# Kernel tuning notes

Hardware: AMD Instinct MI355X
Metric: run time of the kernel (lower is better)

Reference implementation:

```python
import jax, jax.numpy as jnp
import numpy as np

N_EDGES = 262144
N_TRIP = 1048576
D = 128
N_RBF = 6
A_DIM = 49  # n_spher * l_spher
N_BIL = 8


def setup_inputs() -> dict:
    key = jax.random.key(0)
    ks = jax.random.split(key, 16)
    s = lambda fan_in: 1.0 / np.sqrt(fan_in)
    return {
        "m_ji": jax.random.normal(ks[0], (N_EDGES, D), jnp.float32),
        "e_rbf": jax.random.normal(ks[1], (N_EDGES, N_RBF), jnp.float32),
        "a_sbf": jax.random.normal(ks[2], (N_TRIP, A_DIM), jnp.float32),
        "nbr_list": jax.random.randint(ks[3], (N_EDGES, 2), 0, 100000),
        "angle_list": jax.random.randint(ks[4], (N_TRIP, 3), 0, N_EDGES),
        "kj_idx": jax.random.randint(ks[5], (N_TRIP,), 0, N_EDGES),
        "nbr_m_w": jax.random.normal(ks[6], (D, D), jnp.float32) * s(D),
        "nbr_m_b": jnp.zeros((D,), jnp.float32),
        "e_rbf_w": jax.random.normal(ks[7], (N_RBF, D), jnp.float32) * s(N_RBF),
        "a_sbf_w": jax.random.normal(ks[8], (A_DIM, N_BIL), jnp.float32) * s(A_DIM),
        "final_w": jax.random.normal(ks[9], (D, N_BIL, D), jnp.float32) * s(N_BIL * D),
        "m_ji_w": jax.random.normal(ks[10], (D, D), jnp.float32) * s(D),
        "m_ji_b": jnp.zeros((D,), jnp.float32),
        "post_w": jax.random.normal(ks[11], (D, D), jnp.float32) * s(D),
        "post_b": jnp.zeros((D,), jnp.float32),
        "res_w": jax.random.normal(ks[12], (3, 2, D, D), jnp.float32) * s(D),
        "res_b": jnp.zeros((3, 2, D), jnp.float32),
    }


def _residual(x, w2, b2):
    # two Dense(swish) layers + skip
    out = x
    for k in range(2):
        out = jax.nn.silu(out @ w2[k] + b2[k])
    return out + x


def reference(m_ji, e_rbf, a_sbf, nbr_list, angle_list, kj_idx,
              nbr_m_w, nbr_m_b, e_rbf_w, a_sbf_w, final_w,
              m_ji_w, m_ji_b, post_w, post_b, res_w, res_b):
    # DirectedMessage: gather per-triplet edge features
    t_m = jax.nn.silu(m_ji[kj_idx] @ nbr_m_w + nbr_m_b)   # [W, D]
    t_e = e_rbf[kj_idx] @ e_rbf_w                          # [W, D]
    m_and_e = t_m * t_e                                    # [W, D]
    t_a = a_sbf @ a_sbf_w                                  # [W, J]
    out = jnp.einsum('wj,wl,ijl->wi', t_a, m_and_e, final_w)  # [W, D]
    directed = jax.ops.segment_sum(out, kj_idx, num_segments=m_ji.shape[0])  # [E, D]

    transf_m_ji = jax.nn.silu(m_ji @ m_ji_w + m_ji_b)
    output = directed + transf_m_ji
    output = _residual(output, res_w[0], res_b[0])
    output = jax.nn.silu(output @ post_w + post_b) + transf_m_ji
    output = _residual(output, res_w[1], res_b[1])
    output = _residual(output, res_w[2], res_b[2])
    return output
```

## Files before the change

### kernel.cpp

```cpp
#include <hip/hip_runtime.h>

#define N_EDGE 262144
#define N_TRI  1048576
#define DIM    128
#define NRBF   6
#define ADIM   49
#define NBIL   8
#define TE     64
#define NTHR   256
#define SXD    68
#define EB2    2048
#define NSL    4

typedef __attribute__((ext_vector_type(8))) short bf16x8;
typedef __attribute__((ext_vector_type(4))) float f32x4;

__device__ __forceinline__ float fast_rcp(float x) {
    float r; asm("v_rcp_f32 %0, %1" : "=v"(r) : "v"(x)); return r;
}
__device__ __forceinline__ float fast_exp2(float x) {
    float r; asm("v_exp_f32 %0, %1" : "=v"(r) : "v"(x)); return r;
}
__device__ __forceinline__ float silu_f(float x) {
    return x * fast_rcp(1.f + fast_exp2(-1.44269504f * x));
}
__device__ __forceinline__ unsigned short f2bf(float f) {
    unsigned int u = __float_as_uint(f);
    return (unsigned short)((u + 0x7FFFu + ((u >> 16) & 1u)) >> 16);
}
__device__ __forceinline__ unsigned int pk2(float x, float y) {
    unsigned int r;
    asm("v_cvt_pk_bf16_f32 %0, %1, %2" : "=v"(r) : "v"(x), "v"(y));
    return r;
}
__device__ __forceinline__ float bf2f(unsigned short u) {
    return __uint_as_float(((unsigned int)u) << 16);
}

__global__ __launch_bounds__(256) void prep_w_k(
    const float* __restrict__ nbr, const float* __restrict__ mji,
    const float* __restrict__ post, const float* __restrict__ res,
    const float* __restrict__ fw, unsigned short* __restrict__ wt)
{
    int idx = blockIdx.x * 256 + threadIdx.x;
    if (idx < 9 * 16384) {
        int m = idx >> 14, rr = idx & 16383;
        int n = rr >> 7, ks = rr & 127;
        int ko = (ks & ~31) | ((ks & 1) << 4) | ((ks >> 1) & 15);
        const float* src = (m == 0) ? nbr : (m == 1) ? mji : (m == 2) ? post
                          : (res + (size_t)(m - 3) * 16384);
        wt[idx] = f2bf(src[ko * DIM + n]);
    } else {
        int r2 = idx - 9 * 16384;
        int n = r2 >> 10, j = (r2 >> 7) & 7, ls = r2 & 127;
        int lo = (ls & ~31) | ((ls & 1) << 4) | ((ls >> 1) & 15);
        wt[idx] = f2bf(fw[(size_t)(n * NBIL + j) * DIM + lo]);
    }
}

__global__ __launch_bounds__(256) void ta_all_k(
    const float* __restrict__ a_sbf, const float* __restrict__ a_sbf_w,
    float* __restrict__ taw)
{
    __shared__ __align__(16) float sA[256 * ADIM];
    __shared__ float sWa[ADIM * NBIL];
    const int tid = threadIdx.x;
    const size_t w0 = (size_t)blockIdx.x * 256;

    {
        const float4* src = (const float4*)(a_sbf + w0 * ADIM);
        float4* dst = (float4*)sA;
        for (int i = tid; i < (256 * ADIM) / 4; i += 256) dst[i] = src[i];
    }
    for (int i = tid; i < ADIM * NBIL; i += 256) sWa[i] = a_sbf_w[i];
    __syncthreads();

    float ta[NBIL];
    #pragma unroll
    for (int j = 0; j < NBIL; ++j) ta[j] = 0.0f;
    const float* row = sA + tid * ADIM;
    #pragma unroll
    for (int k = 0; k < ADIM; ++k) {
        float v = row[k];
        #pragma unroll
        for (int j = 0; j < NBIL; ++j) ta[j] = fmaf(v, sWa[k * NBIL + j], ta[j]);
    }
    float4* dst = (float4*)(taw + (w0 + tid) * NBIL);
    dst[0] = make_float4(ta[0], ta[1], ta[2], ta[3]);
    dst[1] = make_float4(ta[4], ta[5], ta[6], ta[7]);
}

__global__ __launch_bounds__(1024) void seg_reduce_k(
    const float* __restrict__ taw, const int* __restrict__ kj_idx,
    float* __restrict__ ta_sum)
{
    __shared__ float acc[EB2 * NBIL];
    const int tid = threadIdx.x;
    const int eg = blockIdx.x >> 2;
    const int sl = blockIdx.x & 3;
    const int lo = eg * EB2;

    for (int i = tid; i < EB2 * NBIL; i += 1024) acc[i] = 0.f;
    __syncthreads();

    const int4* kj4 = (const int4*)kj_idx;
    const int i0 = sl * (N_TRI / 4 / NSL);
    const int i1 = i0 + (N_TRI / 4 / NSL);
    for (int i = i0 + tid; i < i1; i += 1024) {
        int4 v = kj4[i];
        int w0 = i * 4;
        #pragma unroll
        for (int k = 0; k < 4; ++k) {
            int e = (k == 0) ? v.x : (k == 1) ? v.y : (k == 2) ? v.z : v.w;
            unsigned d = (unsigned)(e - lo);
            if (d < (unsigned)EB2) {
                const float4* p = (const float4*)(taw + (size_t)(w0 + k) * NBIL);
                float4 a = p[0], b = p[1];
                float* q = acc + d * NBIL;
                atomicAdd(q + 0, a.x); atomicAdd(q + 1, a.y);
                atomicAdd(q + 2, a.z); atomicAdd(q + 3, a.w);
                atomicAdd(q + 4, b.x); atomicAdd(q + 5, b.y);
                atomicAdd(q + 6, b.z); atomicAdd(q + 7, b.w);
            }
        }
    }
    __syncthreads();
    for (int i = tid; i < EB2 * NBIL; i += 1024)
        unsafeAtomicAdd(ta_sum + (size_t)lo * NBIL + i, acc[i]);
}

__global__ __launch_bounds__(256) void triplet_atomic_k(
    const float* __restrict__ a_sbf, const float* __restrict__ a_sbf_w,
    const int* __restrict__ kj_idx, float* __restrict__ ta_sum)
{
    __shared__ __align__(16) float sA[256 * ADIM];
    __shared__ float sWa[ADIM * NBIL];
    const int tid = threadIdx.x;
    const size_t w0 = (size_t)blockIdx.x * 256;
    {
        const float4* src = (const float4*)(a_sbf + w0 * ADIM);
        float4* dst = (float4*)sA;
        for (int i = tid; i < (256 * ADIM) / 4; i += 256) dst[i] = src[i];
    }
    for (int i = tid; i < ADIM * NBIL; i += 256) sWa[i] = a_sbf_w[i];
    __syncthreads();
    float ta[NBIL];
    #pragma unroll
    for (int j = 0; j < NBIL; ++j) ta[j] = 0.0f;
    const float* row = sA + tid * ADIM;
    #pragma unroll
    for (int k = 0; k < ADIM; ++k) {
        float v = row[k];
        #pragma unroll
        for (int j = 0; j < NBIL; ++j) ta[j] = fmaf(v, sWa[k * NBIL + j], ta[j]);
    }
    const int e = kj_idx[w0 + tid];
    float* dst = ta_sum + (size_t)e * NBIL;
    #pragma unroll
    for (int j = 0; j < NBIL; ++j) unsafeAtomicAdd(dst + j, ta[j]);
}

__global__ __launch_bounds__(NTHR) void edge_main_k(
    const float* __restrict__ m_ji, const float* __restrict__ e_rbf,
    const float* __restrict__ ta_sum, const unsigned short* __restrict__ wt,
    const float* __restrict__ nbr_m_b, const float* __restrict__ e_rbf_w,
    const float* __restrict__ m_ji_b, const float* __restrict__ post_b,
    const float* __restrict__ res_b, float* __restrict__ out)
{
    __shared__ __align__(16) unsigned int sXd[TE * SXD];
    __shared__ __align__(16) unsigned int sTd[TE * SXD];
    __shared__ __align__(16) float sTAT[NBIL * TE];
    __shared__ __align__(16) float sET[NRBF * TE];

    const int tid  = threadIdx.x;
    const int lane = tid & 63;
    const int ml   = lane & 15;
    const int g    = lane >> 4;
    const int wq   = tid >> 6;
    const int n0   = wq * 32;
    const int q16  = wq * 16;
    const size_t e0 = (size_t)blockIdx.x * TE;

    bf16x8 A[4][2], Bf[2][4];
    f32x4 acc[4][2], xr[4][2], zac;
    float b0, b1;

    auto prefB = [&](const unsigned short* wtm, int ldk, int kbase) {
        #pragma unroll
        for (int nt = 0; nt < 2; ++nt) {
            const unsigned short* wb =
                wtm + (size_t)(n0 + nt * 16 + ml) * ldk + kbase + g * 8;
            #pragma unroll
            for (int ks = 0; ks < 4; ++ks)
                Bf[nt][ks] = *(const bf16x8*)(wb + ks * 32);
        }
    };
    auto ldbias = [&](const float* bp) {
        b0 = bp[n0 + ml]; b1 = bp[n0 + 16 + ml];
    };

    prefB(wt + 1 * 16384, DIM, 0);
    ldbias(m_ji_b);
    zac[0] = 0.f; zac[1] = 0.f; zac[2] = 0.f; zac[3] = 0.f;

    #pragma unroll
    for (int i = 0; i < 4; ++i) {
        int q = tid + i * NTHR;
        int row = q >> 4, sub = q & 15;
        int dq = sub >> 2, c4 = (sub & 3) * 4;
        const float* src = m_ji + (e0 + row) * DIM + dq * 32 + c4;
        float4 a = *(const float4*)(src);
        float4 b = *(const float4*)(src + 16);
        uint4 d;
        d.x = pk2(a.x, b.x); d.y = pk2(a.y, b.y);
        d.z = pk2(a.z, b.z); d.w = pk2(a.w, b.w);
        *(uint4*)(sXd + row * SXD + dq * 16 + c4) = d;
    }
    #pragma unroll
    for (int i = 0; i < 2; ++i) {
        int idx = tid + i * NTHR;
        int j = idx >> 6, e = idx & 63;
        sTAT[j * TE + e] = ta_sum[(e0 + e) * NBIL + j];
    }
    for (int i = tid; i < NRBF * TE; i += NTHR) {
        int j = i >> 6, e = i & 63;
        sET[j * TE + e] = e_rbf[(e0 + e) * NRBF + j];
    }
    __syncthreads();

    auto loadA = [&](int h) {
        const unsigned short* base = (const unsigned short*)sXd;
        #pragma unroll
        for (int mt = 0; mt < 4; ++mt) {
            const unsigned short* rb = base + (mt * 16 + ml) * (SXD * 2) + h * 64 + g * 8;
            A[mt][0] = *(const bf16x8*)(rb);
            A[mt][1] = *(const bf16x8*)(rb + 32);
        }
    };
    auto mfmaH = [&](int h, bool seed) {
        #pragma unroll
        for (int kk = 0; kk < 2; ++kk)
        #pragma unroll
        for (int nt = 0; nt < 2; ++nt)
        #pragma unroll
        for (int mt = 0; mt < 4; ++mt)
            acc[mt][nt] = __builtin_amdgcn_mfma_f32_16x16x32_bf16(
                A[mt][kk], Bf[nt][h * 2 + kk],
                (seed && kk == 0) ? zac : acc[mt][nt], 0, 0, 0);
    };
    auto gemm_full = [&]() { loadA(0); mfmaH(0, true); loadA(1); mfmaH(1, false); };
    auto store_sX = [&](f32x4 (&v)[4][2]) {
        __syncthreads();
        #pragma unroll
        for (int mt = 0; mt < 4; ++mt)
        #pragma unroll
        for (int r = 0; r < 4; ++r)
            sXd[(mt * 16 + g * 4 + r) * SXD + q16 + ml] = pk2(v[mt][0][r], v[mt][1][r]);
        __syncthreads();
    };

    gemm_full();
    prefB(wt + 0 * 16384, DIM, 0);
    #pragma unroll
    for (int mt = 0; mt < 4; ++mt)
    #pragma unroll
    for (int r = 0; r < 4; ++r)
        sTd[(mt * 16 + g * 4 + r) * SXD + q16 + ml] =
            pk2(silu_f(acc[mt][0][r] + b0), silu_f(acc[mt][1][r] + b1));

    ldbias(nbr_m_b);
    float ewc[2][NRBF];
    #pragma unroll
    for (int nt = 0; nt < 2; ++nt)
    #pragma unroll
    for (int q = 0; q < NRBF; ++q)
        ewc[nt][q] = e_rbf_w[q * DIM + n0 + nt * 16 + ml];
    gemm_full();
    const unsigned short* fwb = wt + 9 * 16384;
    prefB(fwb, NBIL * DIM, 0);
    #pragma unroll
    for (int mt = 0; mt < 4; ++mt) {
        f32x4 er[NRBF];
        #pragma unroll
        for (int q = 0; q < NRBF; ++q)
            er[q] = *(const f32x4*)(sET + q * TE + mt * 16 + g * 4);
        #pragma unroll
        for (int r = 0; r < 4; ++r) {
            float te0 = 0.f, te1 = 0.f;
            #pragma unroll
            for (int q = 0; q < NRBF; ++q) {
                te0 = fmaf(er[q][r], ewc[0][q], te0);
                te1 = fmaf(er[q][r], ewc[1][q], te1);
            }
            acc[mt][0][r] = silu_f(acc[mt][0][r] + b0) * te0;
            acc[mt][1][r] = silu_f(acc[mt][1][r] + b1) * te1;
        }
    }
    store_sX(acc);

    #pragma unroll
    for (int mt = 0; mt < 4; ++mt)
    #pragma unroll
    for (int r = 0; r < 4; ++r) {
        unsigned int t = sTd[(mt * 16 + g * 4 + r) * SXD + q16 + ml];
        xr[mt][0][r] = bf2f((unsigned short)(t & 0xffff));
        xr[mt][1][r] = bf2f((unsigned short)(t >> 16));
    }
    for (int j = 0; j < NBIL; ++j) {
        gemm_full();
        if (j < NBIL - 1) prefB(fwb, NBIL * DIM, (j + 1) * DIM);
        else              prefB(wt + 3 * 16384, DIM, 0);
        #pragma unroll
        for (int mt = 0; mt < 4; ++mt) {
            f32x4 tv = *(const f32x4*)(sTAT + j * TE + mt * 16 + g * 4);
            #pragma unroll
            for (int nt = 0; nt < 2; ++nt)
            #pragma unroll
            for (int r = 0; r < 4; ++r)
                xr[mt][nt][r] = fmaf(tv[r], acc[mt][nt][r], xr[mt][nt][r]);
        }
    }
    store_sX(xr);

    ldbias(res_b + 0);
    gemm_full(); prefB(wt + 4 * 16384, DIM, 0);
    #pragma unroll
    for (int mt = 0; mt < 4; ++mt)
    #pragma unroll
    for (int r = 0; r < 4; ++r) {
        acc[mt][0][r] = silu_f(acc[mt][0][r] + b0);
        acc[mt][1][r] = silu_f(acc[mt][1][r] + b1);
    }
    store_sX(acc);
    ldbias(res_b + 128);
    gemm_full(); prefB(wt + 2 * 16384, DIM, 0);
    #pragma unroll
    for (int mt = 0; mt < 4; ++mt)
    #pragma unroll
    for (int r = 0; r < 4; ++r) {
        xr[mt][0][r] += silu_f(acc[mt][0][r] + b0);
        xr[mt][1][r] += silu_f(acc[mt][1][r] + b1);
    }
    store_sX(xr);

    ldbias(post_b);
    gemm_full(); prefB(wt + 5 * 16384, DIM, 0);
    #pragma unroll
    for (int mt = 0; mt < 4; ++mt)
    #pragma unroll
    for (int r = 0; r < 4; ++r) {
        unsigned int t = sTd[(mt * 16 + g * 4 + r) * SXD + q16 + ml];
        xr[mt][0][r] = silu_f(acc[mt][0][r] + b0) + bf2f((unsigned short)(t & 0xffff));
        xr[mt][1][r] = silu_f(acc[mt][1][r] + b1) + bf2f((unsigned short)(t >> 16));
    }
    store_sX(xr);

    ldbias(res_b + 256);
    gemm_full(); prefB(wt + 6 * 16384, DIM, 0);
    #pragma unroll
    for (int mt = 0; mt < 4; ++mt)
    #pragma unroll
    for (int r = 0; r < 4; ++r) {
        acc[mt][0][r] = silu_f(acc[mt][0][r] + b0);
        acc[mt][1][r] = silu_f(acc[mt][1][r] + b1);
    }
    store_sX(acc);
    ldbias(res_b + 384);
    gemm_full(); prefB(wt + 7 * 16384, DIM, 0);
    #pragma unroll
    for (int mt = 0; mt < 4; ++mt)
    #pragma unroll
    for (int r = 0; r < 4; ++r) {
        xr[mt][0][r] += silu_f(acc[mt][0][r] + b0);
        xr[mt][1][r] += silu_f(acc[mt][1][r] + b1);
    }
    store_sX(xr);

    ldbias(res_b + 512);
    gemm_full(); prefB(wt + 8 * 16384, DIM, 0);
    #pragma unroll
    for (int mt = 0; mt < 4; ++mt)
    #pragma unroll
    for (int r = 0; r < 4; ++r) {
        acc[mt][0][r] = silu_f(acc[mt][0][r] + b0);
        acc[mt][1][r] = silu_f(acc[mt][1][r] + b1);
    }
    store_sX(acc);
    ldbias(res_b + 640);
    gemm_full();
    #pragma unroll
    for (int mt = 0; mt < 4; ++mt)
    #pragma unroll
    for (int r = 0; r < 4; ++r) {
        int row = mt * 16 + g * 4 + r;
        out[(e0 + row) * DIM + n0 + ml]      = silu_f(acc[mt][0][r] + b0) + xr[mt][0][r];
        out[(e0 + row) * DIM + n0 + 16 + ml] = silu_f(acc[mt][1][r] + b1) + xr[mt][1][r];
    }
}

extern "C" void kernel_launch(void* const* d_in, const int* in_sizes, int n_in,
                              void* d_out, int out_size, void* d_ws, size_t ws_size,
                              hipStream_t stream)
{
    (void)in_sizes; (void)n_in; (void)out_size;
    const float* m_ji    = (const float*)d_in[0];
    const float* e_rbf   = (const float*)d_in[1];
    const float* a_sbf   = (const float*)d_in[2];
    const int*   kj_idx  = (const int*)d_in[5];
    const float* nbr_m_w = (const float*)d_in[6];
    const float* nbr_m_b = (const float*)d_in[7];
    const float* e_rbf_w = (const float*)d_in[8];
    const float* a_sbf_w = (const float*)d_in[9];
    const float* final_w = (const float*)d_in[10];
    const float* m_ji_w  = (const float*)d_in[11];
    const float* m_ji_b  = (const float*)d_in[12];
    const float* post_w  = (const float*)d_in[13];
    const float* post_b  = (const float*)d_in[14];
    const float* res_w   = (const float*)d_in[15];
    const float* res_b   = (const float*)d_in[16];
    float* out = (float*)d_out;

    const size_t taB  = (size_t)N_EDGE * NBIL * sizeof(float);
    const size_t wtB  = (size_t)278528 * sizeof(unsigned short);
    const size_t tawB = (size_t)N_TRI * NBIL * sizeof(float);

    float* ta_sum = (float*)d_ws;
    unsigned short* wt = (unsigned short*)((char*)d_ws + taB);
    float* taw = (float*)((char*)d_ws + taB + wtB);

    prep_w_k<<<1088, 256, 0, stream>>>(nbr_m_w, m_ji_w, post_w, res_w, final_w, wt);
    hipMemsetAsync(ta_sum, 0, taB, stream);

    if (ws_size >= taB + wtB + tawB) {
        ta_all_k<<<N_TRI / 256, 256, 0, stream>>>(a_sbf, a_sbf_w, taw);
        seg_reduce_k<<<(N_EDGE / EB2) * NSL, 1024, 0, stream>>>(taw, kj_idx, ta_sum);
    } else {
        triplet_atomic_k<<<N_TRI / 256, 256, 0, stream>>>(a_sbf, a_sbf_w, kj_idx, ta_sum);
    }
    edge_main_k<<<N_EDGE / TE, NTHR, 0, stream>>>(m_ji, e_rbf, ta_sum, wt,
        nbr_m_b, e_rbf_w, m_ji_b, post_b, res_b, out);
}
```

Baseline: 453.3 us.

## Double-buffer LDS activations, seed MFMA with bias, spill skip tensor to output

Replaces the single LDS activation buffer with two ping-pong buffers, so each layer's store needs only one barrier instead of two. Moves the transf_m_ji skip tensor out of LDS into a per-block scratch area in the output buffer, which cuts LDS use and may allow more resident blocks. Biases now seed the MFMA accumulator, removing the per-element bias adds. The cost is global-memory round trips for the skip tensor, whose scratch region is later overwritten by the final output.

```diff
diff --git a/kernel.cpp b/kernel.cpp
--- a/kernel.cpp
+++ b/kernel.cpp
@@ -167,8 +167,7 @@
     const float* __restrict__ m_ji_b, const float* __restrict__ post_b,
     const float* __restrict__ res_b, float* __restrict__ out)
 {
-    __shared__ __align__(16) unsigned int sXd[TE * SXD];
-    __shared__ __align__(16) unsigned int sTd[TE * SXD];
+    __shared__ __align__(16) unsigned int sXd[2][TE * SXD];
     __shared__ __align__(16) float sTAT[NBIL * TE];
     __shared__ __align__(16) float sET[NRBF * TE];
 
@@ -181,9 +180,10 @@
     const int q16  = wq * 16;
     const size_t e0 = (size_t)blockIdx.x * TE;
 
+    unsigned int* tscr = (unsigned int*)(out + e0 * DIM);
+
     bf16x8 A[4][2], Bf[2][4];
-    f32x4 acc[4][2], xr[4][2], zac;
-    float b0, b1;
+    f32x4 acc[4][2], xr[4][2], bs0, bs1;
 
     auto prefB = [&](const unsigned short* wtm, int ldk, int kbase) {
         #pragma unroll
@@ -196,12 +196,16 @@
         }
     };
     auto ldbias = [&](const float* bp) {
-        b0 = bp[n0 + ml]; b1 = bp[n0 + 16 + ml];
+        float b0 = bp[n0 + ml], b1 = bp[n0 + 16 + ml];
+        bs0[0] = b0; bs0[1] = b0; bs0[2] = b0; bs0[3] = b0;
+        bs1[0] = b1; bs1[1] = b1; bs1[2] = b1; bs1[3] = b1;
+    };
+    auto ldzero = [&]() {
+        #pragma unroll
+        for (int r = 0; r < 4; ++r) { bs0[r] = 0.f; bs1[r] = 0.f; }
     };
 
     prefB(wt + 1 * 16384, DIM, 0);
-    ldbias(m_ji_b);
-    zac[0] = 0.f; zac[1] = 0.f; zac[2] = 0.f; zac[3] = 0.f;
 
     #pragma unroll
     for (int i = 0; i < 4; ++i) {
@@ -214,7 +218,7 @@
         uint4 d;
         d.x = pk2(a.x, b.x); d.y = pk2(a.y, b.y);
         d.z = pk2(a.z, b.z); d.w = pk2(a.w, b.w);
-        *(uint4*)(sXd + row * SXD + dq * 16 + c4) = d;
+        *(uint4*)(sXd[0] + row * SXD + dq * 16 + c4) = d;
     }
     #pragma unroll
     for (int i = 0; i < 2; ++i) {
@@ -228,8 +232,8 @@
     }
     __syncthreads();
 
-    auto loadA = [&](int h) {
-        const unsigned short* base = (const unsigned short*)sXd;
+    auto loadA = [&](const unsigned int* bufp, int h) {
+        const unsigned short* base = (const unsigned short*)bufp;
         #pragma unroll
         for (int mt = 0; mt < 4; ++mt) {
             const unsigned short* rb = base + (mt * 16 + ml) * (SXD * 2) + h * 64 + g * 8;
@@ -243,30 +247,36 @@
         #pragma unroll
         for (int nt = 0; nt < 2; ++nt)
         #pragma unroll
+        for (int mt = 0; mt < 4; ++mt) {
+            f32x4 cin = (seed && kk == 0) ? (nt == 0 ? bs0 : bs1) : acc[mt][nt];
+            acc[mt][nt] = __builtin_amdgcn_mfma_f32_16x16x32_bf16(
+                A[mt][kk], Bf[nt][h * 2 + kk], cin, 0, 0, 0);
+        }
+    };
+    auto gemm_full = [&](const unsigned int* bufp) {
+        loadA(bufp, 0); mfmaH(0, true); loadA(bufp, 1); mfmaH(1, false);
+    };
+    auto store_sX = [&](unsigned int* bufp, f32x4 (&v)[4][2]) {
+        #pragma unroll
         for (int mt = 0; mt < 4; ++mt)
-            acc[mt][nt] = __builtin_amdgcn_mfma_f32_16x16x32_bf16(
-                A[mt][kk], Bf[nt][h * 2 + kk],
-                (seed && kk == 0) ? zac : acc[mt][nt], 0, 0, 0);
-    };
-    auto gemm_full = [&]() { loadA(0); mfmaH(0, true); loadA(1); mfmaH(1, false); };
-    auto store_sX = [&](f32x4 (&v)[4][2]) {
+        #pragma unroll
+        for (int r = 0; r < 4; ++r)
+            bufp[(mt * 16 + g * 4 + r) * SXD + q16 + ml] = pk2(v[mt][0][r], v[mt][1][r]);
         __syncthreads();
-        #pragma unroll
-        for (int mt = 0; mt < 4; ++mt)
-        #pragma unroll
-        for (int r = 0; r < 4; ++r)
-            sXd[(mt * 16 + g * 4 + r) * SXD + q16 + ml] = pk2(v[mt][0][r], v[mt][1][r]);
-        __syncthreads();
-    };
-
-    gemm_full();
+    };
+
+    unsigned int* bufA = sXd[0];
+    unsigned int* bufB = sXd[1];
+
+    ldbias(m_ji_b);
+    gemm_full(bufA);
     prefB(wt + 0 * 16384, DIM, 0);
     #pragma unroll
     for (int mt = 0; mt < 4; ++mt)
     #pragma unroll
     for (int r = 0; r < 4; ++r)
-        sTd[(mt * 16 + g * 4 + r) * SXD + q16 + ml] =
-            pk2(silu_f(acc[mt][0][r] + b0), silu_f(acc[mt][1][r] + b1));
+        tscr[(mt * 16 + g * 4 + r) * 64 + q16 + ml] =
+            pk2(silu_f(acc[mt][0][r]), silu_f(acc[mt][1][r]));
 
     ldbias(nbr_m_b);
     float ewc[2][NRBF];
@@ -275,7 +285,7 @@
     #pragma unroll
     for (int q = 0; q < NRBF; ++q)
         ewc[nt][q] = e_rbf_w[q * DIM + n0 + nt * 16 + ml];
-    gemm_full();
+    gemm_full(bufA);
     const unsigned short* fwb = wt + 9 * 16384;
     prefB(fwb, NBIL * DIM, 0);
     #pragma unroll
@@ -292,22 +302,23 @@
                 te0 = fmaf(er[q][r], ewc[0][q], te0);
                 te1 = fmaf(er[q][r], ewc[1][q], te1);
             }
-            acc[mt][0][r] = silu_f(acc[mt][0][r] + b0) * te0;
-            acc[mt][1][r] = silu_f(acc[mt][1][r] + b1) * te1;
-        }
-    }
-    store_sX(acc);
-
-    #pragma unroll
-    for (int mt = 0; mt < 4; ++mt)
-    #pragma unroll
-    for (int r = 0; r < 4; ++r) {
-        unsigned int t = sTd[(mt * 16 + g * 4 + r) * SXD + q16 + ml];
+            acc[mt][0][r] = silu_f(acc[mt][0][r]) * te0;
+            acc[mt][1][r] = silu_f(acc[mt][1][r]) * te1;
+        }
+    }
+    store_sX(bufB, acc);
+
+    #pragma unroll
+    for (int mt = 0; mt < 4; ++mt)
+    #pragma unroll
+    for (int r = 0; r < 4; ++r) {
+        unsigned int t = tscr[(mt * 16 + g * 4 + r) * 64 + q16 + ml];
         xr[mt][0][r] = bf2f((unsigned short)(t & 0xffff));
         xr[mt][1][r] = bf2f((unsigned short)(t >> 16));
     }
+    ldzero();
     for (int j = 0; j < NBIL; ++j) {
-        gemm_full();
+        gemm_full(bufB);
         if (j < NBIL - 1) prefB(fwb, NBIL * DIM, (j + 1) * DIM);
         else              prefB(wt + 3 * 16384, DIM, 0);
         #pragma unroll
@@ -320,81 +331,81 @@
                 xr[mt][nt][r] = fmaf(tv[r], acc[mt][nt][r], xr[mt][nt][r]);
         }
     }
-    store_sX(xr);
+    store_sX(bufA, xr);
 
     ldbias(res_b + 0);
-    gemm_full(); prefB(wt + 4 * 16384, DIM, 0);
-    #pragma unroll
-    for (int mt = 0; mt < 4; ++mt)
-    #pragma unroll
-    for (int r = 0; r < 4; ++r) {
-        acc[mt][0][r] = silu_f(acc[mt][0][r] + b0);
-        acc[mt][1][r] = silu_f(acc[mt][1][r] + b1);
-    }
-    store_sX(acc);
+    gemm_full(bufA); prefB(wt + 4 * 16384, DIM, 0);
+    #pragma unroll
+    for (int mt = 0; mt < 4; ++mt)
+    #pragma unroll
+    for (int r = 0; r < 4; ++r) {
+        acc[mt][0][r] = silu_f(acc[mt][0][r]);
+        acc[mt][1][r] = silu_f(acc[mt][1][r]);
+    }
+    store_sX(bufB, acc);
     ldbias(res_b + 128);
-    gemm_full(); prefB(wt + 2 * 16384, DIM, 0);
-    #pragma unroll
-    for (int mt = 0; mt < 4; ++mt)
-    #pragma unroll
-    for (int r = 0; r < 4; ++r) {
-        xr[mt][0][r] += silu_f(acc[mt][0][r] + b0);
-        xr[mt][1][r] += silu_f(acc[mt][1][r] + b1);
-    }
-    store_sX(xr);
+    gemm_full(bufB); prefB(wt + 2 * 16384, DIM, 0);
+    #pragma unroll
+    for (int mt = 0; mt < 4; ++mt)
+    #pragma unroll
+    for (int r = 0; r < 4; ++r) {
+        xr[mt][0][r] += silu_f(acc[mt][0][r]);
+        xr[mt][1][r] += silu_f(acc[mt][1][r]);
+    }
+    store_sX(bufA, xr);
 
     ldbias(post_b);
-    gemm_full(); prefB(wt + 5 * 16384, DIM, 0);
-    #pragma unroll
-    for (int mt = 0; mt < 4; ++mt)
-    #pragma unroll
-    for (int r = 0; r < 4; ++r) {
-        unsigned int t = sTd[(mt * 16 + g * 4 + r) * SXD + q16 + ml];
-        xr[mt][0][r] = silu_f(acc[mt][0][r] + b0) + bf2f((unsigned short)(t & 0xffff));
-        xr[mt][1][r] = silu_f(acc[mt][1][r] + b1) + bf2f((unsigned short)(t >> 16));
-    }
-    store_sX(xr);
+    gemm_full(bufA); prefB(wt + 5 * 16384, DIM, 0);
+    #pragma unroll
+    for (int mt = 0; mt < 4; ++mt)
+    #pragma unroll
+    for (int r = 0; r < 4; ++r) {
+        unsigned int t = tscr[(mt * 16 + g * 4 + r) * 64 + q16 + ml];
+        xr[mt][0][r] = silu_f(acc[mt][0][r]) + bf2f((unsigned short)(t & 0xffff));
+        xr[mt][1][r] = silu_f(acc[mt][1][r]) + bf2f((unsigned short)(t >> 16));
+    }
+    store_sX(bufB, xr);
 
     ldbias(res_b + 256);
-    gemm_full(); prefB(wt + 6 * 16384, DIM, 0);
-    #pragma unroll
-    for (int mt = 0; mt < 4; ++mt)
-    #pragma unroll
-    for (int r = 0; r < 4; ++r) {
-        acc[mt][0][r] = silu_f(acc[mt][0][r] + b0);
-        acc[mt][1][r] = silu_f(acc[mt][1][r] + b1);
-    }
-    store_sX(acc);
+    gemm_full(bufB); prefB(wt + 6 * 16384, DIM, 0);
+    #pragma unroll
+    for (int mt = 0; mt < 4; ++mt)
+    #pragma unroll
+    for (int r = 0; r < 4; ++r) {
+        acc[mt][0][r] = silu_f(acc[mt][0][r]);
+        acc[mt][1][r] = silu_f(acc[mt][1][r]);
+    }
+    store_sX(bufA, acc);
     ldbias(res_b + 384);
-    gemm_full(); prefB(wt + 7 * 16384, DIM, 0);
-    #pragma unroll
-    for (int mt = 0; mt < 4; ++mt)
-    #pragma unroll
-    for (int r = 0; r < 4; ++r) {
-        xr[mt][0][r] += silu_f(acc[mt][0][r] + b0);
-        xr[mt][1][r] += silu_f(acc[mt][1][r] + b1);
-    }
-    store_sX(xr);
+    gemm_full(bufA); prefB(wt + 7 * 16384, DIM, 0);
+    #pragma unroll
+    for (int mt = 0; mt < 4; ++mt)
+    #pragma unroll
+    for (int r = 0; r < 4; ++r) {
+        xr[mt][0][r] += silu_f(acc[mt][0][r]);
+        xr[mt][1][r] += silu_f(acc[mt][1][r]);
+    }
+    store_sX(bufB, xr);
 
     ldbias(res_b + 512);
-    gemm_full(); prefB(wt + 8 * 16384, DIM, 0);
-    #pragma unroll
-    for (int mt = 0; mt < 4; ++mt)
-    #pragma unroll
-    for (int r = 0; r < 4; ++r) {
-        acc[mt][0][r] = silu_f(acc[mt][0][r] + b0);
-        acc[mt][1][r] = silu_f(acc[mt][1][r] + b1);
-    }
-    store_sX(acc);
+    gemm_full(bufB); prefB(wt + 8 * 16384, DIM, 0);
+    #pragma unroll
+    for (int mt = 0; mt < 4; ++mt)
+    #pragma unroll
+    for (int r = 0; r < 4; ++r) {
+        acc[mt][0][r] = silu_f(acc[mt][0][r]);
+        acc[mt][1][r] = silu_f(acc[mt][1][r]);
+    }
+    store_sX(bufA, acc);
     ldbias(res_b + 640);
-    gemm_full();
+    gemm_full(bufA);
     #pragma unroll
     for (int mt = 0; mt < 4; ++mt)
     #pragma unroll
     for (int r = 0; r < 4; ++r) {
         int row = mt * 16 + g * 4 + r;
-        out[(e0 + row) * DIM + n0 + ml]      = silu_f(acc[mt][0][r] + b0) + xr[mt][0][r];
-        out[(e0 + row) * DIM + n0 + 16 + ml] = silu_f(acc[mt][1][r] + b1) + xr[mt][1][r];
+        out[(e0 + row) * DIM + n0 + ml]      = silu_f(acc[mt][0][r]) + xr[mt][0][r];
+        out[(e0 + row) * DIM + n0 + 16 + ml] = silu_f(acc[mt][1][r]) + xr[mt][1][r];
     }
 }
 
```

Result: slower. 539.1 us (+18.9%).

## Reuse A fragments across bilinear loop and fold bias into MFMA seed

Applied to the files above, without the earlier changes.

Reorders the bilinear j-loop to iterate over K-halves outermost, so each A half is loaded from LDS once and reused for all eight final_w slices, with half-width B prefetch. Bias is now broadcast into the MFMA accumulator seed, which removes the per-element bias adds in every epilogue. The nbr_m GEMM starts with the A half left in registers by the previous GEMM, skipping one LDS load. The trade-offs are more register pressure from the broadcast bias vectors and partial-sum accumulation into xr across halves.

```diff
diff --git a/kernel.cpp b/kernel.cpp
--- a/kernel.cpp
+++ b/kernel.cpp
@@ -182,8 +182,7 @@
     const size_t e0 = (size_t)blockIdx.x * TE;
 
     bf16x8 A[4][2], Bf[2][4];
-    f32x4 acc[4][2], xr[4][2], zac;
-    float b0, b1;
+    f32x4 acc[4][2], xr[4][2], bs0, bs1;
 
     auto prefB = [&](const unsigned short* wtm, int ldk, int kbase) {
         #pragma unroll
@@ -195,13 +194,27 @@
                 Bf[nt][ks] = *(const bf16x8*)(wb + ks * 32);
         }
     };
+    auto prefBh = [&](const unsigned short* wtm, int ldk, int kbase, int h) {
+        #pragma unroll
+        for (int nt = 0; nt < 2; ++nt) {
+            const unsigned short* wb =
+                wtm + (size_t)(n0 + nt * 16 + ml) * ldk + kbase + g * 8;
+            #pragma unroll
+            for (int kk = 0; kk < 2; ++kk)
+                Bf[nt][h * 2 + kk] = *(const bf16x8*)(wb + (h * 2 + kk) * 32);
+        }
+    };
     auto ldbias = [&](const float* bp) {
-        b0 = bp[n0 + ml]; b1 = bp[n0 + 16 + ml];
+        float b0 = bp[n0 + ml], b1 = bp[n0 + 16 + ml];
+        bs0[0] = b0; bs0[1] = b0; bs0[2] = b0; bs0[3] = b0;
+        bs1[0] = b1; bs1[1] = b1; bs1[2] = b1; bs1[3] = b1;
+    };
+    auto ldzero = [&]() {
+        #pragma unroll
+        for (int r = 0; r < 4; ++r) { bs0[r] = 0.f; bs1[r] = 0.f; }
     };
 
     prefB(wt + 1 * 16384, DIM, 0);
-    ldbias(m_ji_b);
-    zac[0] = 0.f; zac[1] = 0.f; zac[2] = 0.f; zac[3] = 0.f;
 
     #pragma unroll
     for (int i = 0; i < 4; ++i) {
@@ -243,10 +256,11 @@
         #pragma unroll
         for (int nt = 0; nt < 2; ++nt)
         #pragma unroll
-        for (int mt = 0; mt < 4; ++mt)
+        for (int mt = 0; mt < 4; ++mt) {
+            f32x4 cin = (seed && kk == 0) ? (nt == 0 ? bs0 : bs1) : acc[mt][nt];
             acc[mt][nt] = __builtin_amdgcn_mfma_f32_16x16x32_bf16(
-                A[mt][kk], Bf[nt][h * 2 + kk],
-                (seed && kk == 0) ? zac : acc[mt][nt], 0, 0, 0);
+                A[mt][kk], Bf[nt][h * 2 + kk], cin, 0, 0, 0);
+        }
     };
     auto gemm_full = [&]() { loadA(0); mfmaH(0, true); loadA(1); mfmaH(1, false); };
     auto store_sX = [&](f32x4 (&v)[4][2]) {
@@ -259,6 +273,7 @@
         __syncthreads();
     };
 
+    ldbias(m_ji_b);
     gemm_full();
     prefB(wt + 0 * 16384, DIM, 0);
     #pragma unroll
@@ -266,7 +281,7 @@
     #pragma unroll
     for (int r = 0; r < 4; ++r)
         sTd[(mt * 16 + g * 4 + r) * SXD + q16 + ml] =
-            pk2(silu_f(acc[mt][0][r] + b0), silu_f(acc[mt][1][r] + b1));
+            pk2(silu_f(acc[mt][0][r]), silu_f(acc[mt][1][r]));
 
     ldbias(nbr_m_b);
     float ewc[2][NRBF];
@@ -275,7 +290,9 @@
     #pragma unroll
     for (int q = 0; q < NRBF; ++q)
         ewc[nt][q] = e_rbf_w[q * DIM + n0 + nt * 16 + ml];
-    gemm_full();
+    mfmaH(1, true);
+    loadA(0);
+    mfmaH(0, false);
     const unsigned short* fwb = wt + 9 * 16384;
     prefB(fwb, NBIL * DIM, 0);
     #pragma unroll
@@ -292,8 +309,8 @@
                 te0 = fmaf(er[q][r], ewc[0][q], te0);
                 te1 = fmaf(er[q][r], ewc[1][q], te1);
             }
-            acc[mt][0][r] = silu_f(acc[mt][0][r] + b0) * te0;
-            acc[mt][1][r] = silu_f(acc[mt][1][r] + b1) * te1;
+            acc[mt][0][r] = silu_f(acc[mt][0][r]) * te0;
+            acc[mt][1][r] = silu_f(acc[mt][1][r]) * te1;
         }
     }
     store_sX(acc);
@@ -306,18 +323,24 @@
         xr[mt][0][r] = bf2f((unsigned short)(t & 0xffff));
         xr[mt][1][r] = bf2f((unsigned short)(t >> 16));
     }
-    for (int j = 0; j < NBIL; ++j) {
-        gemm_full();
-        if (j < NBIL - 1) prefB(fwb, NBIL * DIM, (j + 1) * DIM);
-        else              prefB(wt + 3 * 16384, DIM, 0);
-        #pragma unroll
-        for (int mt = 0; mt < 4; ++mt) {
-            f32x4 tv = *(const f32x4*)(sTAT + j * TE + mt * 16 + g * 4);
+    ldzero();
+    #pragma unroll
+    for (int h = 0; h < 2; ++h) {
+        loadA(h);
+        for (int j = 0; j < NBIL; ++j) {
+            mfmaH(h, true);
+            if (j < NBIL - 1)      prefBh(fwb, NBIL * DIM, (j + 1) * DIM, h);
+            else if (h == 0)       prefBh(fwb, NBIL * DIM, 0, 1);
+            else                   prefB(wt + 3 * 16384, DIM, 0);
             #pragma unroll
-            for (int nt = 0; nt < 2; ++nt)
-            #pragma unroll
-            for (int r = 0; r < 4; ++r)
-                xr[mt][nt][r] = fmaf(tv[r], acc[mt][nt][r], xr[mt][nt][r]);
+            for (int mt = 0; mt < 4; ++mt) {
+                f32x4 tv = *(const f32x4*)(sTAT + j * TE + mt * 16 + g * 4);
+                #pragma unroll
+                for (int nt = 0; nt < 2; ++nt)
+                #pragma unroll
+                for (int r = 0; r < 4; ++r)
+                    xr[mt][nt][r] = fmaf(tv[r], acc[mt][nt][r], xr[mt][nt][r]);
+            }
         }
     }
     store_sX(xr);
@@ -328,8 +351,8 @@
     for (int mt = 0; mt < 4; ++mt)
     #pragma unroll
     for (int r = 0; r < 4; ++r) {
-        acc[mt][0][r] = silu_f(acc[mt][0][r] + b0);
-        acc[mt][1][r] = silu_f(acc[mt][1][r] + b1);
+        acc[mt][0][r] = silu_f(acc[mt][0][r]);
+        acc[mt][1][r] = silu_f(acc[mt][1][r]);
     }
     store_sX(acc);
     ldbias(res_b + 128);
@@ -338,8 +361,8 @@
     for (int mt = 0; mt < 4; ++mt)
     #pragma unroll
     for (int r = 0; r < 4; ++r) {
-        xr[mt][0][r] += silu_f(acc[mt][0][r] + b0);
-        xr[mt][1][r] += silu_f(acc[mt][1][r] + b1);
+        xr[mt][0][r] += silu_f(acc[mt][0][r]);
+        xr[mt][1][r] += silu_f(acc[mt][1][r]);
     }
     store_sX(xr);
 
@@ -350,8 +373,8 @@
     #pragma unroll
     for (int r = 0; r < 4; ++r) {
         unsigned int t = sTd[(mt * 16 + g * 4 + r) * SXD + q16 + ml];
-        xr[mt][0][r] = silu_f(acc[mt][0][r] + b0) + bf2f((unsigned short)(t & 0xffff));
-        xr[mt][1][r] = silu_f(acc[mt][1][r] + b1) + bf2f((unsigned short)(t >> 16));
+        xr[mt][0][r] = silu_f(acc[mt][0][r]) + bf2f((unsigned short)(t & 0xffff));
+        xr[mt][1][r] = silu_f(acc[mt][1][r]) + bf2f((unsigned short)(t >> 16));
     }
     store_sX(xr);
 
@@ -361,8 +384,8 @@
     for (int mt = 0; mt < 4; ++mt)
     #pragma unroll
     for (int r = 0; r < 4; ++r) {
-        acc[mt][0][r] = silu_f(acc[mt][0][r] + b0);
-        acc[mt][1][r] = silu_f(acc[mt][1][r] + b1);
+        acc[mt][0][r] = silu_f(acc[mt][0][r]);
+        acc[mt][1][r] = silu_f(acc[mt][1][r]);
     }
     store_sX(acc);
     ldbias(res_b + 384);
@@ -371,8 +394,8 @@
     for (int mt = 0; mt < 4; ++mt)
     #pragma unroll
     for (int r = 0; r < 4; ++r) {
-        xr[mt][0][r] += silu_f(acc[mt][0][r] + b0);
-        xr[mt][1][r] += silu_f(acc[mt][1][r] + b1);
+        xr[mt][0][r] += silu_f(acc[mt][0][r]);
+        xr[mt][1][r] += silu_f(acc[mt][1][r]);
     }
     store_sX(xr);
 
@@ -382,8 +405,8 @@
     for (int mt = 0; mt < 4; ++mt)
     #pragma unroll
     for (int r = 0; r < 4; ++r) {
-        acc[mt][0][r] = silu_f(acc[mt][0][r] + b0);
-        acc[mt][1][r] = silu_f(acc[mt][1][r] + b1);
+        acc[mt][0][r] = silu_f(acc[mt][0][r]);
+        acc[mt][1][r] = silu_f(acc[mt][1][r]);
     }
     store_sX(acc);
     ldbias(res_b + 640);
@@ -393,8 +416,8 @@
     #pragma unroll
     for (int r = 0; r < 4; ++r) {
         int row = mt * 16 + g * 4 + r;
-        out[(e0 + row) * DIM + n0 + ml]      = silu_f(acc[mt][0][r] + b0) + xr[mt][0][r];
-        out[(e0 + row) * DIM + n0 + 16 + ml] = silu_f(acc[mt][1][r] + b1) + xr[mt][1][r];
+        out[(e0 + row) * DIM + n0 + ml]      = silu_f(acc[mt][0][r]) + xr[mt][0][r];
+        out[(e0 + row) * DIM + n0 + 16 + ml] = silu_f(acc[mt][1][r]) + xr[mt][1][r];
     }
 }
 
```

Measured after the change: 803.7 us. +77.3%, slower.

## Retile edge kernel waves to 32x64 output tiles with streamed B fragments

Applied to the files above, without the earlier changes.

Each wave now computes a 32-row by 64-column tile instead of all 64 rows by 32 columns. The A fragment for the full K is loaded once per stage from LDS, and the weight fragments are streamed per 16-column slice with double buffering. Bias is folded into the MFMA accumulator seed, and cross-stage B prefetch is replaced by in-stage loads. This cuts LDS A-fragment reads per wave and balances the A/B fragment load per MFMA. The cost is that global weight loads are exposed at the start of each stage rather than prefetched during the previous epilogue.

```diff
diff --git a/kernel.cpp b/kernel.cpp
--- a/kernel.cpp
+++ b/kernel.cpp
@@ -176,32 +176,27 @@
     const int lane = tid & 63;
     const int ml   = lane & 15;
     const int g    = lane >> 4;
-    const int wq   = tid >> 6;
-    const int n0   = wq * 32;
-    const int q16  = wq * 16;
+    const int wid  = tid >> 6;
+    const int mb   = (wid >> 1) * 32;
+    const int n0   = (wid & 1) * 64;
+    const int dq0  = n0 >> 1;
     const size_t e0 = (size_t)blockIdx.x * TE;
 
-    bf16x8 A[4][2], Bf[2][4];
-    f32x4 acc[4][2], xr[4][2], zac;
-    float b0, b1;
-
-    auto prefB = [&](const unsigned short* wtm, int ldk, int kbase) {
-        #pragma unroll
-        for (int nt = 0; nt < 2; ++nt) {
-            const unsigned short* wb =
-                wtm + (size_t)(n0 + nt * 16 + ml) * ldk + kbase + g * 8;
-            #pragma unroll
-            for (int ks = 0; ks < 4; ++ks)
-                Bf[nt][ks] = *(const bf16x8*)(wb + ks * 32);
-        }
+    bf16x8 A[2][4], Bb[2][4];
+    f32x4 acc[2][4], xr[2][4];
+    float bv[4];
+
+    auto loadB = [&](int p, const unsigned short* wtm, int ldk, int nt, int kbase) {
+        const unsigned short* wb =
+            wtm + (size_t)(n0 + nt * 16 + ml) * ldk + kbase + g * 8;
+        #pragma unroll
+        for (int ks = 0; ks < 4; ++ks)
+            Bb[p][ks] = *(const bf16x8*)(wb + ks * 32);
     };
     auto ldbias = [&](const float* bp) {
-        b0 = bp[n0 + ml]; b1 = bp[n0 + 16 + ml];
+        #pragma unroll
+        for (int nt = 0; nt < 4; ++nt) bv[nt] = bp[n0 + nt * 16 + ml];
     };
-
-    prefB(wt + 1 * 16384, DIM, 0);
-    ldbias(m_ji_b);
-    zac[0] = 0.f; zac[1] = 0.f; zac[2] = 0.f; zac[3] = 0.f;
 
     #pragma unroll
     for (int i = 0; i < 4; ++i) {
@@ -228,173 +223,201 @@
     }
     __syncthreads();
 
-    auto loadA = [&](int h) {
+    auto loadA = [&]() {
         const unsigned short* base = (const unsigned short*)sXd;
         #pragma unroll
-        for (int mt = 0; mt < 4; ++mt) {
-            const unsigned short* rb = base + (mt * 16 + ml) * (SXD * 2) + h * 64 + g * 8;
-            A[mt][0] = *(const bf16x8*)(rb);
-            A[mt][1] = *(const bf16x8*)(rb + 32);
+        for (int mt = 0; mt < 2; ++mt) {
+            const unsigned short* rb = base + (mb + mt * 16 + ml) * (SXD * 2) + g * 8;
+            #pragma unroll
+            for (int ks = 0; ks < 4; ++ks)
+                A[mt][ks] = *(const bf16x8*)(rb + ks * 32);
         }
     };
-    auto mfmaH = [&](int h, bool seed) {
-        #pragma unroll
-        for (int kk = 0; kk < 2; ++kk)
-        #pragma unroll
-        for (int nt = 0; nt < 2; ++nt)
-        #pragma unroll
-        for (int mt = 0; mt < 4; ++mt)
-            acc[mt][nt] = __builtin_amdgcn_mfma_f32_16x16x32_bf16(
-                A[mt][kk], Bf[nt][h * 2 + kk],
-                (seed && kk == 0) ? zac : acc[mt][nt], 0, 0, 0);
+    auto gemm_stage = [&](const unsigned short* wtm, int ldk, int kbase) {
+        loadB(0, wtm, ldk, 0, kbase);
+        #pragma unroll
+        for (int nt = 0; nt < 4; ++nt) {
+            const int cur = nt & 1, nxt = cur ^ 1;
+            if (nt < 3) loadB(nxt, wtm, ldk, nt + 1, kbase);
+            f32x4 seed;
+            #pragma unroll
+            for (int r = 0; r < 4; ++r) seed[r] = bv[nt];
+            #pragma unroll
+            for (int mt = 0; mt < 2; ++mt) {
+                f32x4 c = __builtin_amdgcn_mfma_f32_16x16x32_bf16(
+                    A[mt][0], Bb[cur][0], seed, 0, 0, 0);
+                #pragma unroll
+                for (int ks = 1; ks < 4; ++ks)
+                    c = __builtin_amdgcn_mfma_f32_16x16x32_bf16(
+                        A[mt][ks], Bb[cur][ks], c, 0, 0, 0);
+                acc[mt][nt] = c;
+            }
+        }
     };
-    auto gemm_full = [&]() { loadA(0); mfmaH(0, true); loadA(1); mfmaH(1, false); };
-    auto store_sX = [&](f32x4 (&v)[4][2]) {
+    auto store_sX = [&](f32x4 (&v)[2][4]) {
         __syncthreads();
         #pragma unroll
-        for (int mt = 0; mt < 4; ++mt)
-        #pragma unroll
-        for (int r = 0; r < 4; ++r)
-            sXd[(mt * 16 + g * 4 + r) * SXD + q16 + ml] = pk2(v[mt][0][r], v[mt][1][r]);
+        for (int mt = 0; mt < 2; ++mt)
+        #pragma unroll
+        for (int r = 0; r < 4; ++r) {
+            int base = (mb + mt * 16 + g * 4 + r) * SXD + dq0 + ml;
+            sXd[base]      = pk2(v[mt][0][r], v[mt][1][r]);
+            sXd[base + 16] = pk2(v[mt][2][r], v[mt][3][r]);
+        }
         __syncthreads();
     };
 
-    gemm_full();
-    prefB(wt + 0 * 16384, DIM, 0);
-    #pragma unroll
-    for (int mt = 0; mt < 4; ++mt)
-    #pragma unroll
-    for (int r = 0; r < 4; ++r)
-        sTd[(mt * 16 + g * 4 + r) * SXD + q16 + ml] =
-            pk2(silu_f(acc[mt][0][r] + b0), silu_f(acc[mt][1][r] + b1));
+    loadA();
+    ldbias(m_ji_b);
+    gemm_stage(wt + 1 * 16384, DIM, 0);
+    #pragma unroll
+    for (int mt = 0; mt < 2; ++mt)
+    #pragma unroll
+    for (int r = 0; r < 4; ++r) {
+        int base = (mb + mt * 16 + g * 4 + r) * SXD + dq0 + ml;
+        sTd[base]      = pk2(silu_f(acc[mt][0][r]), silu_f(acc[mt][1][r]));
+        sTd[base + 16] = pk2(silu_f(acc[mt][2][r]), silu_f(acc[mt][3][r]));
+    }
 
     ldbias(nbr_m_b);
-    float ewc[2][NRBF];
-    #pragma unroll
-    for (int nt = 0; nt < 2; ++nt)
-    #pragma unroll
-    for (int q = 0; q < NRBF; ++q)
-        ewc[nt][q] = e_rbf_w[q * DIM + n0 + nt * 16 + ml];
-    gemm_full();
+    gemm_stage(wt + 0 * 16384, DIM, 0);
+    {
+        float ewc[4][NRBF];
+        #pragma unroll
+        for (int nt = 0; nt < 4; ++nt)
+        #pragma unroll
+        for (int q = 0; q < NRBF; ++q)
+            ewc[nt][q] = e_rbf_w[q * DIM + n0 + nt * 16 + ml];
+        #pragma unroll
+        for (int mt = 0; mt < 2; ++mt) {
+            f32x4 er[NRBF];
+            #pragma unroll
+            for (int q = 0; q < NRBF; ++q)
+                er[q] = *(const f32x4*)(sET + q * TE + mb + mt * 16 + g * 4);
+            #pragma unroll
+            for (int r = 0; r < 4; ++r)
+            #pragma unroll
+            for (int nt = 0; nt < 4; ++nt) {
+                float te = 0.f;
+                #pragma unroll
+                for (int q = 0; q < NRBF; ++q) te = fmaf(er[q][r], ewc[nt][q], te);
+                acc[mt][nt][r] = silu_f(acc[mt][nt][r]) * te;
+            }
+        }
+    }
+    store_sX(acc);
+
+    loadA();
+    #pragma unroll
+    for (int mt = 0; mt < 2; ++mt)
+    #pragma unroll
+    for (int r = 0; r < 4; ++r) {
+        int base = (mb + mt * 16 + g * 4 + r) * SXD + dq0 + ml;
+        unsigned int t0 = sTd[base], t1 = sTd[base + 16];
+        xr[mt][0][r] = bf2f((unsigned short)(t0 & 0xffff));
+        xr[mt][1][r] = bf2f((unsigned short)(t0 >> 16));
+        xr[mt][2][r] = bf2f((unsigned short)(t1 & 0xffff));
+        xr[mt][3][r] = bf2f((unsigned short)(t1 >> 16));
+    }
     const unsigned short* fwb = wt + 9 * 16384;
-    prefB(fwb, NBIL * DIM, 0);
-    #pragma unroll
-    for (int mt = 0; mt < 4; ++mt) {
-        f32x4 er[NRBF];
-        #pragma unroll
-        for (int q = 0; q < NRBF; ++q)
-            er[q] = *(const f32x4*)(sET + q * TE + mt * 16 + g * 4);
-        #pragma unroll
-        for (int r = 0; r < 4; ++r) {
-            float te0 = 0.f, te1 = 0.f;
-            #pragma unroll
-            for (int q = 0; q < NRBF; ++q) {
-                te0 = fmaf(er[q][r], ewc[0][q], te0);
-                te1 = fmaf(er[q][r], ewc[1][q], te1);
+    for (int j = 0; j < NBIL; ++j) {
+        f32x4 tv[2];
+        #pragma unroll
+        for (int mt = 0; mt < 2; ++mt)
+            tv[mt] = *(const f32x4*)(sTAT + j * TE + mb + mt * 16 + g * 4);
+        loadB(0, fwb, NBIL * DIM, 0, j * DIM);
+        #pragma unroll
+        for (int nt = 0; nt < 4; ++nt) {
+            const int cur = nt & 1, nxt = cur ^ 1;
+            if (nt < 3) loadB(nxt, fwb, NBIL * DIM, nt + 1, j * DIM);
+            #pragma unroll
+            for (int mt = 0; mt < 2; ++mt) {
+                f32x4 c = {0.f, 0.f, 0.f, 0.f};
+                c = __builtin_amdgcn_mfma_f32_16x16x32_bf16(A[mt][0], Bb[cur][0], c, 0, 0, 0);
+                #pragma unroll
+                for (int ks = 1; ks < 4; ++ks)
+                    c = __builtin_amdgcn_mfma_f32_16x16x32_bf16(A[mt][ks], Bb[cur][ks], c, 0, 0, 0);
+                #pragma unroll
+                for (int r = 0; r < 4; ++r)
+                    xr[mt][nt][r] = fmaf(tv[mt][r], c[r], xr[mt][nt][r]);
             }
-            acc[mt][0][r] = silu_f(acc[mt][0][r] + b0) * te0;
-            acc[mt][1][r] = silu_f(acc[mt][1][r] + b1) * te1;
-        }
-    }
+        }
+    }
+    store_sX(xr);
+
+    loadA(); ldbias(res_b + 0);
+    gemm_stage(wt + 3 * 16384, DIM, 0);
+    #pragma unroll
+    for (int mt = 0; mt < 2; ++mt)
+    #pragma unroll
+    for (int nt = 0; nt < 4; ++nt)
+    #pragma unroll
+    for (int r = 0; r < 4; ++r) acc[mt][nt][r] = silu_f(acc[mt][nt][r]);
     store_sX(acc);
-
-    #pragma unroll
-    for (int mt = 0; mt < 4; ++mt)
+    loadA(); ldbias(res_b + 128);
+    gemm_stage(wt + 4 * 16384, DIM, 0);
+    #pragma unroll
+    for (int mt = 0; mt < 2; ++mt)
+    #pragma unroll
+    for (int nt = 0; nt < 4; ++nt)
+    #pragma unroll
+    for (int r = 0; r < 4; ++r) xr[mt][nt][r] += silu_f(acc[mt][nt][r]);
+    store_sX(xr);
+
+    loadA(); ldbias(post_b);
+    gemm_stage(wt + 2 * 16384, DIM, 0);
+    #pragma unroll
+    for (int mt = 0; mt < 2; ++mt)
     #pragma unroll
     for (int r = 0; r < 4; ++r) {
-        unsigned int t = sTd[(mt * 16 + g * 4 + r) * SXD + q16 + ml];
-        xr[mt][0][r] = bf2f((unsigned short)(t & 0xffff));
-        xr[mt][1][r] = bf2f((unsigned short)(t >> 16));
-    }
-    for (int j = 0; j < NBIL; ++j) {
-        gemm_full();
-        if (j < NBIL - 1) prefB(fwb, NBIL * DIM, (j + 1) * DIM);
-        else              prefB(wt + 3 * 16384, DIM, 0);
-        #pragma unroll
-        for (int mt = 0; mt < 4; ++mt) {
-            f32x4 tv = *(const f32x4*)(sTAT + j * TE + mt * 16 + g * 4);
-            #pragma unroll
-            for (int nt = 0; nt < 2; ++nt)
-            #pragma unroll
-            for (int r = 0; r < 4; ++r)
-                xr[mt][nt][r] = fmaf(tv[r], acc[mt][nt][r], xr[mt][nt][r]);
-        }
+        int base = (mb + mt * 16 + g * 4 + r) * SXD + dq0 + ml;
+        unsigned int t0 = sTd[base], t1 = sTd[base + 16];
+        xr[mt][0][r] = silu_f(acc[mt][0][r]) + bf2f((unsigned short)(t0 & 0xffff));
+        xr[mt][1][r] = silu_f(acc[mt][1][r]) + bf2f((unsigned short)(t0 >> 16));
+        xr[mt][2][r] = silu_f(acc[mt][2][r]) + bf2f((unsigned short)(t1 & 0xffff));
+        xr[mt][3][r] = silu_f(acc[mt][3][r]) + bf2f((unsigned short)(t1 >> 16));
     }
     store_sX(xr);
 
-    ldbias(res_b + 0);
-    gemm_full(); prefB(wt + 4 * 16384, DIM, 0);
-    #pragma unroll
-    for (int mt = 0; mt < 4; ++mt)
+    loadA(); ldbias(res_b + 256);
+    gemm_stage(wt + 5 * 16384, DIM, 0);
+    #pragma unroll
+    for (int mt = 0; mt < 2; ++mt)
+    #pragma unroll
+    for (int nt = 0; nt < 4; ++nt)
+    #pragma unroll
+    for (int r = 0; r < 4; ++r) acc[mt][nt][r] = silu_f(acc[mt][nt][r]);
+    store_sX(acc);
+    loadA(); ldbias(res_b + 384);
+    gemm_stage(wt + 6 * 16384, DIM, 0);
+    #pragma unroll
+    for (int mt = 0; mt < 2; ++mt)
+    #pragma unroll
+    for (int nt = 0; nt < 4; ++nt)
+    #pragma unroll
+    for (int r = 0; r < 4; ++r) xr[mt][nt][r] += silu_f(acc[mt][nt][r]);
+    store_sX(xr);
+
+    loadA(); ldbias(res_b + 512);
+    gemm_stage(wt + 7 * 16384, DIM, 0);
+    #pragma unroll
+    for (int mt = 0; mt < 2; ++mt)
+    #pragma unroll
+    for (int nt = 0; nt < 4; ++nt)
+    #pragma unroll
+    for (int r = 0; r < 4; ++r) acc[mt][nt][r] = silu_f(acc[mt][nt][r]);
+    store_sX(acc);
+    loadA(); ldbias(res_b + 640);
+    gemm_stage(wt + 8 * 16384, DIM, 0);
+    #pragma unroll
+    for (int mt = 0; mt < 2; ++mt)
     #pragma unroll
     for (int r = 0; r < 4; ++r) {
-        acc[mt][0][r] = silu_f(acc[mt][0][r] + b0);
-        acc[mt][1][r] = silu_f(acc[mt][1][r] + b1);
-    }
-    store_sX(acc);
-    ldbias(res_b + 128);
-    gemm_full(); prefB(wt + 2 * 16384, DIM, 0);
-    #pragma unroll
-    for (int mt = 0; mt < 4; ++mt)
-    #pragma unroll
-    for (int r = 0; r < 4; ++r) {
-        xr[mt][0][r] += silu_f(acc[mt][0][r] + b0);
-        xr[mt][1][r] += silu_f(acc[mt][1][r] + b1);
-    }
-    store_sX(xr);
-
-    ldbias(post_b);
-    gemm_full(); prefB(wt + 5 * 16384, DIM, 0);
-    #pragma unroll
-    for (int mt = 0; mt < 4; ++mt)
-    #pragma unroll
-    for (int r = 0; r < 4; ++r) {
-        unsigned int t = sTd[(mt * 16 + g * 4 + r) * SXD + q16 + ml];
-        xr[mt][0][r] = silu_f(acc[mt][0][r] + b0) + bf2f((unsigned short)(t & 0xffff));
-        xr[mt][1][r] = silu_f(acc[mt][1][r] + b1) + bf2f((unsigned short)(t >> 16));
-    }
-    store_sX(xr);
-
-    ldbias(res_b + 256);
-    gemm_full(); prefB(wt + 6 * 16384, DIM, 0);
-    #pragma unroll
-    for (int mt = 0; mt < 4; ++mt)
-    #pragma unroll
-    for (int r = 0; r < 4; ++r) {
-        acc[mt][0][r] = silu_f(acc[mt][0][r] + b0);
-        acc[mt][1][r] = silu_f(acc[mt][1][r] + b1);
-    }
-    store_sX(acc);
-    ldbias(res_b + 384);
-    gemm_full(); prefB(wt + 7 * 16384, DIM, 0);
-    #pragma unroll
-    for (int mt = 0; mt < 4; ++mt)
-    #pragma unroll
-    for (int r = 0; r < 4; ++r) {
-        xr[mt][0][r] += silu_f(acc[mt][0][r] + b0);
-        xr[mt][1][r] += silu_f(acc[mt][1][r] + b1);
-    }
-    store_sX(xr);
-
-    ldbias(res_b + 512);
-    gemm_full(); prefB(wt + 8 * 16384, DIM, 0);
-    #pragma unroll
-    for (int mt = 0; mt < 4; ++mt)
-    #pragma unroll
-    for (int r = 0; r < 4; ++r) {
-        acc[mt][0][r] = silu_f(acc[mt][0][r] + b0);
-        acc[mt][1][r] = silu_f(acc[mt][1][r] + b1);
-    }
-    store_sX(acc);
-    ldbias(res_b + 640);
-    gemm_full();
-    #pragma unroll
-    for (int mt = 0; mt < 4; ++mt)
-    #pragma unroll
-    for (int r = 0; r < 4; ++r) {
-        int row = mt * 16 + g * 4 + r;
-        out[(e0 + row) * DIM + n0 + ml]      = silu_f(acc[mt][0][r] + b0) + xr[mt][0][r];
-        out[(e0 + row) * DIM + n0 + 16 + ml] = silu_f(acc[mt][1][r] + b1) + xr[mt][1][r];
+        int row = mb + mt * 16 + g * 4 + r;
+        #pragma unroll
+        for (int nt = 0; nt < 4; ++nt)
+            out[(e0 + row) * DIM + n0 + nt * 16 + ml] =
+                silu_f(acc[mt][nt][r]) + xr[mt][nt][r];
     }
 }
 
```

Result: slower. 801.6 us (+76.8%).
